# Optimization experiments

Hardware: AMD Instinct MI355X
Metric: run time of the kernel (lower is better)

The kernel has to match this reference:

```python
import jax, jax.numpy as jnp
import numpy as np

EPS = 1e-5      # batch-norm epsilon
ALPHA = 0.2     # leaky_relu negative slope


def bn_lrelu(h, gamma, beta):
    # training-mode batch norm over the batch axis, then leaky relu
    mean = jnp.mean(h, axis=0)
    var = jnp.var(h, axis=0)
    h = (h - mean) * jax.lax.rsqrt(var + EPS) * gamma + beta
    return jnp.where(h >= 0, h, ALPHA * h)


def setup_inputs() -> dict:
    key = jax.random.key(0)
    ks = jax.random.split(key, 16)
    O, T, Din, H, Dout = 50000, 200000, 128, 512, 128
    s = 0.02
    inp = {
        "obj_vecs": jax.random.normal(ks[0], (O, Din), jnp.float32),
        "pred_vecs": jax.random.normal(ks[1], (T, Din), jnp.float32),
        "edges": jax.random.randint(ks[2], (T, 2), 0, O, jnp.int64),
        # net1: [3*Din -> H -> 2H+Dout], each Linear followed by BN + leaky_relu
        "W1a": jax.random.normal(ks[3], (3 * Din, H), jnp.float32) * s,
        "b1a": jnp.zeros((H,), jnp.float32),
        "g1a": jnp.ones((H,), jnp.float32),
        "be1a": jnp.zeros((H,), jnp.float32),
        "W1b": jax.random.normal(ks[4], (H, 2 * H + Dout), jnp.float32) * s,
        "b1b": jnp.zeros((2 * H + Dout,), jnp.float32),
        "g1b": jnp.ones((2 * H + Dout,), jnp.float32),
        "be1b": jnp.zeros((2 * H + Dout,), jnp.float32),
        # net2: [H -> H -> Dout]
        "W2a": jax.random.normal(ks[5], (H, H), jnp.float32) * s,
        "b2a": jnp.zeros((H,), jnp.float32),
        "g2a": jnp.ones((H,), jnp.float32),
        "be2a": jnp.zeros((H,), jnp.float32),
        "W2b": jax.random.normal(ks[6], (H, Dout), jnp.float32) * s,
        "b2b": jnp.zeros((Dout,), jnp.float32),
        "g2b": jnp.ones((Dout,), jnp.float32),
        "be2b": jnp.zeros((Dout,), jnp.float32),
    }
    return inp


def reference(obj_vecs, pred_vecs, edges,
              W1a, b1a, g1a, be1a, W1b, b1b, g1b, be1b,
              W2a, b2a, g2a, be2a, W2b, b2b, g2b, be2b):
    O = obj_vecs.shape[0]
    H = W1a.shape[1]
    Dout = W2b.shape[1]
    s_idx = edges[:, 0]
    o_idx = edges[:, 1]

    # gather subject/object vecs and concat with predicate vecs: [T, 3*Din]
    cur_t = jnp.concatenate([obj_vecs[s_idx], pred_vecs, obj_vecs[o_idx]], axis=1)

    # net1 MLP
    h = bn_lrelu(cur_t @ W1a + b1a, g1a, be1a)           # [T, H]
    new_t = bn_lrelu(h @ W1b + b1b, g1b, be1b)            # [T, 2H+Dout]

    new_s = new_t[:, :H]
    new_p = new_t[:, H:H + Dout]
    new_o = new_t[:, H + Dout:]

    # scatter-add pooling back to objects, then average
    pooled = jnp.zeros((O, H), jnp.float32).at[s_idx].add(new_s).at[o_idx].add(new_o)
    counts = jnp.zeros((O,), jnp.float32).at[s_idx].add(1.0).at[o_idx].add(1.0)
    counts = jnp.clip(counts, 1.0, float(O))
    pooled = pooled / counts[:, None]

    # net2 MLP
    h2 = bn_lrelu(pooled @ W2a + b2a, g2a, be2a)          # [O, H]
    new_obj = bn_lrelu(h2 @ W2b + b2b, g2b, be2b)         # [O, Dout]
    return new_obj, new_p
```

## Files before the change

### kernel.cpp

```cpp
#include <hip/hip_runtime.h>

typedef __bf16 bf16;
typedef __bf16 bf16x8 __attribute__((ext_vector_type(8)));
typedef float  f32x4  __attribute__((ext_vector_type(4)));

#define BM 128
#define BN 128
#define BKT 64
#define LDK (BKT + 8)
#define LDT 72

template<int AMODE, int EPI>
__global__ __launch_bounds__(256) void gemm_k(
    const bf16* __restrict__ Abf, const float* __restrict__ Af32,
    const float* __restrict__ obj, const float* __restrict__ pred,
    const int* __restrict__ edges, const float* __restrict__ invcnt,
    const float* __restrict__ scale, const float* __restrict__ shift,
    const float* __restrict__ oscale, const float* __restrict__ oshift,
    const bf16* __restrict__ WT,
    bf16* __restrict__ outB, float* __restrict__ outF,
    float* __restrict__ pooled, float* __restrict__ gsum, float* __restrict__ gsq,
    int M, int N, int K)
{
  __shared__ __align__(16) bf16 As[BM][LDK];
  __shared__ __align__(16) bf16 Bs[BN][LDK];
  __shared__ float sc_sh[(AMODE == 1) ? 512 : 1];
  __shared__ float sh_sh[(AMODE == 1) ? 512 : 1];
  __shared__ float osc[(EPI == 2) ? BN : 1];
  __shared__ float osh[(EPI == 2) ? BN : 1];
  __shared__ int eS[(AMODE == 0 || EPI == 2) ? BM : 1];
  __shared__ int eO[(AMODE == 0 || EPI == 2) ? BM : 1];

  const int tid = threadIdx.x;
  const int m0 = blockIdx.y * BM;
  const int n0 = blockIdx.x * BN;
  const int lane = tid & 63;
  const int w = tid >> 6;
  const int wm = (w >> 1) * 64;
  const int wn = (w & 1) * 64;
  const int l15 = lane & 15;
  const int quad = lane >> 4;

  if (AMODE == 1) {
    for (int c = tid; c < K; c += 256) { sc_sh[c] = scale[c]; sh_sh[c] = shift[c]; }
  }
  if (EPI == 2) {
    if (tid < BN) { osc[tid] = oscale[n0 + tid]; osh[tid] = oshift[n0 + tid]; }
  }
  if (AMODE == 0 || EPI == 2) {
    if (tid < BM) {
      int r = m0 + tid; if (r >= M) r = M - 1;
      eS[tid] = edges[2 * r];
      eO[tid] = edges[2 * r + 1];
    }
  }
  __syncthreads();

  f32x4 acc[4][4];
  #pragma unroll
  for (int i = 0; i < 4; ++i)
    #pragma unroll
    for (int j = 0; j < 4; ++j)
      acc[i][j] = (f32x4){0.f, 0.f, 0.f, 0.f};

  for (int k0 = 0; k0 < K; k0 += BKT) {
    {
      int idx = tid;
      #pragma unroll
      for (int it = 0; it < 4; ++it, idx += 256) {
        int r = idx >> 3, c8 = (idx & 7) << 3;
        bf16x8 v = *reinterpret_cast<const bf16x8*>(WT + (size_t)(n0 + r) * K + k0 + c8);
        *reinterpret_cast<bf16x8*>(&Bs[r][c8]) = v;
      }
    }
    if (AMODE == 1 || AMODE == 3) {
      int idx = tid;
      #pragma unroll
      for (int it = 0; it < 4; ++it, idx += 256) {
        int r = idx >> 3, c8 = (idx & 7) << 3;
        int row = m0 + r; if (row >= M) row = M - 1;
        bf16x8 v = *reinterpret_cast<const bf16x8*>(Abf + (size_t)row * K + k0 + c8);
        if (AMODE == 1) {
          bf16x8 o;
          #pragma unroll
          for (int e = 0; e < 8; ++e) {
            int c = k0 + c8 + e;
            float f = sc_sh[c] * (float)v[e] + sh_sh[c];
            f = f >= 0.f ? f : 0.2f * f;
            o[e] = (bf16)f;
          }
          *reinterpret_cast<bf16x8*>(&As[r][c8]) = o;
        } else {
          *reinterpret_cast<bf16x8*>(&As[r][c8]) = v;
        }
      }
    } else {
      int idx = tid;
      #pragma unroll
      for (int it = 0; it < 8; ++it, idx += 256) {
        int r = idx >> 4, c4 = (idx & 15) << 2;
        int row = m0 + r; if (row >= M) row = M - 1;
        const float* src;
        float mul = 1.f;
        if (AMODE == 0) {
          int k = k0 + c4;
          if (k < 128)      src = obj  + (size_t)eS[r] * 128 + k;
          else if (k < 256) src = pred + (size_t)row * 128 + (k - 128);
          else              src = obj  + (size_t)eO[r] * 128 + (k - 256);
        } else {
          src = Af32 + (size_t)row * K + k0 + c4;
          mul = invcnt[row];
        }
        float4 v = *reinterpret_cast<const float4*>(src);
        As[r][c4 + 0] = (bf16)(v.x * mul);
// ... 11 lines not shown
        af[i] = *reinterpret_cast<const bf16x8*>(&As[wm + i * 16 + l15][kk + quad * 8]);
      #pragma unroll
      for (int j = 0; j < 4; ++j)
        bfv[j] = *reinterpret_cast<const bf16x8*>(&Bs[wn + j * 16 + l15][kk + quad * 8]);
      #pragma unroll
      for (int i = 0; i < 4; ++i)
        #pragma unroll
        for (int j = 0; j < 4; ++j)
          acc[i][j] = __builtin_amdgcn_mfma_f32_16x16x32_bf16(af[i], bfv[j], acc[i][j], 0, 0, 0);
    }
    __syncthreads();
  }

  if (EPI == 2) {
    #pragma unroll
    for (int i = 0; i < 4; ++i) {
      #pragma unroll
      for (int r = 0; r < 4; ++r) {
        int lrow = wm + i * 16 + quad * 4 + r;
        int row = m0 + lrow;
        if (row >= M) continue;
        #pragma unroll
        for (int j = 0; j < 4; ++j) {
          int cl = wn + j * 16 + l15;
          int n1 = n0 + cl;
          float v = osc[cl] * acc[i][j][r] + osh[cl];
          v = v >= 0.f ? v : 0.2f * v;
          if (n1 < 512)      atomicAdd(&pooled[(size_t)eS[lrow] * 512 + n1], v);
          else if (n1 < 640) outF[(size_t)row * 128 + (n1 - 512)] = v;
          else               atomicAdd(&pooled[(size_t)eO[lrow] * 512 + (n1 - 640)], v);
        }
      }
    }
  } else {
    #pragma unroll
    for (int j = 0; j < 4; ++j) {
      float s = 0.f, q = 0.f;
      #pragma unroll
      for (int i = 0; i < 4; ++i) {
        #pragma unroll
        for (int r = 0; r < 4; ++r) {
          int row = m0 + wm + i * 16 + quad * 4 + r;
          if (row >= M) continue;
          float v = acc[i][j][r];
          s += v; q += v * v;
          int col = n0 + wn + j * 16 + l15;
          if (EPI == 0) outB[(size_t)row * N + col] = (bf16)v;
          if (EPI == 3) outF[(size_t)row * N + col] = v;
        }
      }
      s += __shfl_xor(s, 16); q += __shfl_xor(q, 16);
      s += __shfl_xor(s, 32); q += __shfl_xor(q, 32);
      if (quad == 0) {
        int col = n0 + wn + j * 16 + l15;
        atomicAdd(&gsum[col], s);
        atomicAdd(&gsq[col], q);
      }
    }
  }
}

__global__ __launch_bounds__(256) void gram_k(const bf16* __restrict__ A2,
                                              float* __restrict__ G, int T) {
  __shared__ __align__(16) bf16 Ks[2][128][LDT];
  const int tid = threadIdx.x;
  const int tile = blockIdx.x & 15;
  const int s    = blockIdx.x >> 4;
  const int NS   = gridDim.x >> 4;
  const int k1b = tile >> 2, k2b = tile & 3;
  const int lane = tid & 63;
  const int w = tid >> 6;
  const int wm = (w >> 1) * 64;
  const int wn = (w & 1) * 64;
  const int l15 = lane & 15;
  const int quad = lane >> 4;

  const int NG = (T + 63) >> 6;
  const int GPB = (NG + NS - 1) / NS;
  const int g0 = s * GPB;
  const int gend = min(NG, g0 + GPB);

  f32x4 acc[4][4];
  #pragma unroll
  for (int i = 0; i < 4; ++i)
    #pragma unroll
    for (int j = 0; j < 4; ++j)
      acc[i][j] = (f32x4){0.f, 0.f, 0.f, 0.f};

  const int bsel = (k1b == k2b) ? 0 : 1;

  for (int g = g0; g < gend; ++g) {
    const int t0 = g << 6;
    #pragma unroll
    for (int it = 0; it < 4; ++it) {
      int lin = it * 256 + tid;
      int t = lin >> 4, c8 = lin & 15;
      int row = t0 + t;
      bf16x8 v;
      #pragma unroll
      for (int e = 0; e < 8; ++e) v[e] = (bf16)0.f;
      if (row < T)
        v = *reinterpret_cast<const bf16x8*>(A2 + (size_t)row * 512 + k1b * 128 + c8 * 8);
// ... 20 lines not shown
    __syncthreads();
    #pragma unroll
    for (int kk = 0; kk < 64; kk += 32) {
      bf16x8 af[4], bfv[4];
      #pragma unroll
      for (int i = 0; i < 4; ++i) {
        int r = wm + i * 16 + l15;
        int toff = (kk + quad * 8) ^ (((r >> 3) & 7) << 3);
        af[i] = *reinterpret_cast<const bf16x8*>(&Ks[0][r][toff]);
      }
      #pragma unroll
      for (int j = 0; j < 4; ++j) {
        int r = wn + j * 16 + l15;
        int toff = (kk + quad * 8) ^ (((r >> 3) & 7) << 3);
        bfv[j] = *reinterpret_cast<const bf16x8*>(&Ks[bsel][r][toff]);
      }
      #pragma unroll
      for (int i = 0; i < 4; ++i)
        #pragma unroll
        for (int j = 0; j < 4; ++j)
          acc[i][j] = __builtin_amdgcn_mfma_f32_16x16x32_bf16(af[i], bfv[j], acc[i][j], 0, 0, 0);
    }
    __syncthreads();
  }

  #pragma unroll
  for (int i = 0; i < 4; ++i) {
    #pragma unroll
    for (int r = 0; r < 4; ++r) {
      int grow = k1b * 128 + wm + i * 16 + quad * 4 + r;
      #pragma unroll
      for (int j = 0; j < 4; ++j) {
        int gcol = k2b * 128 + wn + j * 16 + l15;
        atomicAdd(&G[(size_t)grow * 512 + gcol], acc[i][j][r]);
      }
    }
  }
}

__global__ __launch_bounds__(256) void act_colsum_k(bf16* __restrict__ hA,
    const float* __restrict__ scale, const float* __restrict__ shift,
    float* __restrict__ csum, int T) {
  __shared__ float sh[4 * 512];
  const int tid = threadIdx.x;
  const int c0 = (tid & 63) * 8;
  const int rofs = tid >> 6;
  float sc[8], sf[8];
  #pragma unroll
  for (int j = 0; j < 8; ++j) { sc[j] = scale[c0 + j]; sf[j] = shift[c0 + j]; }
  float acc[8];
  #pragma unroll
  for (int j = 0; j < 8; ++j) acc[j] = 0.f;
  for (int r = blockIdx.x * 4 + rofs; r < T; r += gridDim.x * 4) {
    bf16x8 v = *reinterpret_cast<const bf16x8*>(hA + (size_t)r * 512 + c0);
    bf16x8 o;
    #pragma unroll
    for (int j = 0; j < 8; ++j) {
      float f = sc[j] * (float)v[j] + sf[j];
      f = f >= 0.f ? f : 0.2f * f;
      o[j] = (bf16)f;
      acc[j] += (float)o[j];
    }
    *reinterpret_cast<bf16x8*>(hA + (size_t)r * 512 + c0) = o;
  }
  #pragma unroll
  for (int j = 0; j < 8; ++j) sh[rofs * 512 + c0 + j] = acc[j];
  __syncthreads();
// ... 41 lines not shown
    #pragma unroll
    for (int c = 0; c < 4; ++c) { rq[w][c] = pq[c]; rs[w][c] = ps[c]; }
  }
  __syncthreads();
  if (tid < 4) {
    sqB[c0 + tid]  = rq[0][tid] + rq[1][tid] + rq[2][tid] + rq[3][tid];
    sumB[c0 + tid] = rs[0][tid] + rs[1][tid] + rs[2][tid] + rs[3][tid];
  }
}

__global__ __launch_bounds__(256) void tconv_k(const float* __restrict__ W,
                                               bf16* __restrict__ WT, int K, int N) {
  int idx = blockIdx.x * 256 + threadIdx.x;
  if (idx < K * N) {
    int n = idx / K, k = idx - n * K;
    WT[(size_t)n * K + k] = (bf16)W[(size_t)k * N + n];
  }
}

__global__ __launch_bounds__(256) void bnfin_k(const float* __restrict__ sum,
    const float* __restrict__ sq, const float* __restrict__ g,
    const float* __restrict__ be, float* __restrict__ scale,
    float* __restrict__ shift, int C, float invR) {
  int c = blockIdx.x * 256 + threadIdx.x;
  if (c < C) {
    float m = sum[c] * invR;
    float v = sq[c] * invR - m * m;
    float a = g[c] * rsqrtf(v + 1e-5f);
    scale[c] = a;
    shift[c] = be[c] - m * a;
  }
}

__global__ __launch_bounds__(256) void cntint_k(const int* __restrict__ edges,
                                                int* __restrict__ cnt, int T) {
  int t = blockIdx.x * 256 + threadIdx.x;
  if (t < T) {
    atomicAdd(&cnt[edges[2 * t]], 1);
    atomicAdd(&cnt[edges[2 * t + 1]], 1);
  }
}

__global__ __launch_bounds__(256) void invcnt_k(const int* __restrict__ cnt,
                                                float* __restrict__ invc, int O) {
  int i = blockIdx.x * 256 + threadIdx.x;
  if (i < O) {
    float c = fminf(fmaxf((float)cnt[i], 1.f), (float)O);
    invc[i] = 1.f / c;
  }
}

__global__ __launch_bounds__(1024) void scan_k(const int* __restrict__ cnt,
    int* __restrict__ rowptr, int* __restrict__ head, int O, int total) {
  __shared__ int sh[1024];
  const int t = threadIdx.x;
  const int C = (O + 1023) / 1024;
  const int i0 = t * C;
  int s = 0;
  for (int i = 0; i < C; ++i) { int idx = i0 + i; if (idx < O) s += cnt[idx]; }
  sh[t] = s;
  __syncthreads();
  for (int d = 1; d < 1024; d <<= 1) {
    int v = (t >= d) ? sh[t - d] : 0;
    __syncthreads();
    sh[t] += v;
    __syncthreads();
  }
  int run = (t == 0) ? 0 : sh[t - 1];
  for (int i = 0; i < C; ++i) {
    int idx = i0 + i;
    if (idx < O) { rowptr[idx] = run; head[idx] = run; run += cnt[idx]; }
  }
  if (t == 0) rowptr[O] = total;
}

__global__ __launch_bounds__(256) void fill_k(const int* __restrict__ edges,
    int* __restrict__ head, int* __restrict__ list, int T) {
  int t = blockIdx.x * 256 + threadIdx.x;
  if (t < T) {
    int s = edges[2 * t];
    int p = atomicAdd(&head[s], 1);
    list[p] = t << 1;
    int o = edges[2 * t + 1];
    p = atomicAdd(&head[o], 1);
    list[p] = (t << 1) | 1;
  }
}

__global__ __launch_bounds__(256) void act_k(bf16* __restrict__ hA,
    const float* __restrict__ scale, const float* __restrict__ shift, size_t n8) {
  size_t i = (size_t)blockIdx.x * 256 + threadIdx.x;
  if (i < n8) {
    size_t idx8 = i * 8;
    int c = (int)(idx8 & 511);
    bf16x8 v = *reinterpret_cast<const bf16x8*>(hA + idx8);
    bf16x8 o;
    #pragma unroll
    for (int j = 0; j < 8; ++j) {
      float f = scale[c + j] * (float)v[j] + shift[c + j];
      f = f >= 0.f ? f : 0.2f * f;
      o[j] = (bf16)f;
    }
    *reinterpret_cast<bf16x8*>(hA + idx8) = o;
  }
}

__global__ __launch_bounds__(256) void newp_k(const bf16* __restrict__ tB,
    const float* __restrict__ scale, const float* __restrict__ shift,
    float* __restrict__ outP, int T) {
  int i = blockIdx.x * 256 + threadIdx.x;
  if (i < T * 128) {
    int t = i >> 7, c = i & 127;
    float v = scale[512 + c] * (float)tB[(size_t)t * 1152 + 512 + c] + shift[512 + c];
    outP[i] = v >= 0.f ? v : 0.2f * v;
  }
}

__global__ __launch_bounds__(256) void gather_k(const bf16* __restrict__ tB,
    const int* __restrict__ rowptr, const int* __restrict__ list,
    const float* __restrict__ scale, const float* __restrict__ shift,
    const float* __restrict__ invc, bf16* __restrict__ pooled, int O) {
  int o = blockIdx.x * 4 + (threadIdx.x >> 6);
  if (o >= O) return;
  int lane = threadIdx.x & 63;
  int c0 = lane * 8;
  float scS[8], shS[8], scO[8], shO[8];
  #pragma unroll
  for (int j = 0; j < 8; ++j) {
    scS[j] = scale[c0 + j];       shS[j] = shift[c0 + j];
    scO[j] = scale[640 + c0 + j]; shO[j] = shift[640 + c0 + j];
  }
  float acc[8];
  #pragma unroll
  for (int j = 0; j < 8; ++j) acc[j] = 0.f;
  int e0 = rowptr[o], e1 = rowptr[o + 1];
  for (int e = e0; e < e1; ++e) {
    int id = list[e];
    int t = id >> 1;
    int role = id & 1;
    const bf16* row = tB + (size_t)t * 1152 + (role ? 640 : 0) + c0;
    bf16x8 v = *reinterpret_cast<const bf16x8*>(row);
    if (role) {
      #pragma unroll
      for (int j = 0; j < 8; ++j) {
        float f = scO[j] * (float)v[j] + shO[j];
        acc[j] += (f >= 0.f ? f : 0.2f * f);
      }
    } else {
      #pragma unroll
      for (int j = 0; j < 8; ++j) {
        float f = scS[j] * (float)v[j] + shS[j];
        acc[j] += (f >= 0.f ? f : 0.2f * f);
      }
    }
  }
  float ic = invc[o];
  bf16x8 out;
  #pragma unroll
  for (int j = 0; j < 8; ++j) out[j] = (bf16)(acc[j] * ic);
  *reinterpret_cast<bf16x8*>(pooled + (size_t)o * 512 + c0) = out;
}

__global__ __launch_bounds__(256) void final_k(float* __restrict__ buf,
    const float* __restrict__ scale, const float* __restrict__ shift, int n) {
  int i = blockIdx.x * 256 + threadIdx.x;
  if (i < n) {
    int c = i & 127;
    float v = scale[c] * buf[i] + shift[c];
    buf[i] = v >= 0.f ? v : 0.2f * v;
  }
}

extern "C" void kernel_launch(void* const* d_in, const int* in_sizes, int n_in,
                              void* d_out, int out_size, void* d_ws, size_t ws_size,
                              hipStream_t stream) {
  const float* obj   = (const float*)d_in[0];
  const float* pred  = (const float*)d_in[1];
  const int*   edges = (const int*)d_in[2];
  const float* W1a = (const float*)d_in[3];
  const float* g1a = (const float*)d_in[5];
  const float* be1a= (const float*)d_in[6];
  const float* W1b = (const float*)d_in[7];
  const float* g1b = (const float*)d_in[9];
  const float* be1b= (const float*)d_in[10];
  const float* W2a = (const float*)d_in[11];
  const float* g2a = (const float*)d_in[13];
  const float* be2a= (const float*)d_in[14];
  const float* W2b = (const float*)d_in[15];
  const float* g2b = (const float*)d_in[17];
  const float* be2b= (const float*)d_in[18];

  const int O = in_sizes[0] / 128;
  const int T = in_sizes[1] / 128;
  float* out_obj = (float*)d_out;
  float* out_p   = (float*)d_out + (size_t)O * 128;

  char* base = (char*)d_ws;
  size_t off = 0;
  auto alloc = [&](size_t bytes) { size_t p = off; off += (bytes + 255) & ~(size_t)255; return p; };
  size_t oWT1a = alloc((size_t)384 * 512 * 2);
  size_t oWT1b = alloc((size_t)512 * 1152 * 2);
  size_t oWT2a = alloc((size_t)512 * 512 * 2);
  size_t oWT2b = alloc((size_t)512 * 128 * 2);
  size_t oSums = alloc(4608 * 4);
  size_t oScl  = alloc(4608 * 4);
  size_t oG    = alloc((size_t)512 * 512 * 4);
  size_t oCsum = alloc(512 * 4);
  size_t oCntI = alloc((size_t)O * 4);
  size_t oInvc = alloc((size_t)O * 4);
  size_t oRp   = alloc((size_t)(O + 1) * 4);
  size_t oHead = alloc((size_t)O * 4);
  size_t oList = alloc((size_t)2 * T * 4);
  size_t oHA   = alloc((size_t)T * 512 * 2);
  size_t oBig  = off;
  size_t need_staged = oBig + (((size_t)T * 1152 * 2 + 255) & ~(size_t)255)
                            + (size_t)O * 512 * 2;
  const bool staged = (ws_size >= need_staged);

  bf16* WT1a = (bf16*)(base + oWT1a);
  bf16* WT1b = (bf16*)(base + oWT1b);
  bf16* WT2a = (bf16*)(base + oWT2a);
  bf16* WT2b = (bf16*)(base + oWT2b);
  float* sums = (float*)(base + oSums);
  float* sumA = sums,        * sqA = sums + 512;
  float* sumB = sums + 1024, * sqB = sums + 2176;
  float* sumC = sums + 3328, * sqC = sums + 3840;
  float* sumD = sums + 4352, * sqD = sums + 4480;
  float* scl = (float*)(base + oScl);
  float* scaleA = scl,        * shiftA = scl + 512;
  float* scaleB = scl + 1024, * shiftB = scl + 2176;
  float* scaleC = scl + 3328, * shiftC = scl + 3840;
  float* scaleD = scl + 4352, * shiftD = scl + 4480;
  float* Gm   = (float*)(base + oG);
  float* csum = (float*)(base + oCsum);
  int*   cntI = (int*)(base + oCntI);
  float* invc = (float*)(base + oInvc);
  int*   rowptr = (int*)(base + oRp);
  int*   head = (int*)(base + oHead);
  int*   list = (int*)(base + oList);
  bf16*  hA = (bf16*)(base + oHA);
  bf16*  h2 = (bf16*)(base + oHA);
  bf16*  tB = (bf16*)(base + oBig);
  bf16*  pooledB = (bf16*)(base + oBig + (((size_t)T * 1152 * 2 + 255) & ~(size_t)255));
  float* pooledF = (float*)(base + oBig);
  float* objpre = out_obj;

  hipMemsetAsync(sums, 0, 4608 * 4, stream);
  hipMemsetAsync(cntI, 0, (size_t)O * 4, stream);
  if (!staged) {
    hipMemsetAsync(Gm, 0, (size_t)512 * 512 * 4, stream);
    hipMemsetAsync(csum, 0, 512 * 4, stream);
  }

  tconv_k<<<(384 * 512 + 255) / 256, 256, 0, stream>>>(W1a, WT1a, 384, 512);
  tconv_k<<<(512 * 1152 + 255) / 256, 256, 0, stream>>>(W1b, WT1b, 512, 1152);
  tconv_k<<<(512 * 512 + 255) / 256, 256, 0, stream>>>(W2a, WT2a, 512, 512);
  tconv_k<<<(512 * 128 + 255) / 256, 256, 0, stream>>>(W2b, WT2b, 512, 128);
  cntint_k<<<(T + 255) / 256, 256, 0, stream>>>(edges, cntI, T);
  invcnt_k<<<(O + 255) / 256, 256, 0, stream>>>(cntI, invc, O);
  if (staged) {
    scan_k<<<1, 1024, 0, stream>>>(cntI, rowptr, head, O, 2 * T);
    fill_k<<<(T + 255) / 256, 256, 0, stream>>>(edges, head, list, T);
  }

  const int Tb = (T + BM - 1) / BM;
  const int Ob = (O + BM - 1) / BM;

  {
    dim3 g(512 / BN, Tb);
    gemm_k<0, 0><<<g, 256, 0, stream>>>(nullptr, nullptr, obj, pred, edges, nullptr,
        nullptr, nullptr, nullptr, nullptr, WT1a, hA, nullptr, nullptr, sumA, sqA,
        T, 512, 384);
  }
  bnfin_k<<<2, 256, 0, stream>>>(sumA, sqA, g1a, be1a, scaleA, shiftA, 512, 1.f / T);

  if (staged) {
    act_k<<<(int)(((size_t)T * 512 / 8 + 255) / 256), 256, 0, stream>>>(hA, scaleA,
        shiftA, (size_t)T * 512 / 8);
    {
      dim3 g(1152 / BN, Tb);
      gemm_k<3, 0><<<g, 256, 0, stream>>>(hA, nullptr, nullptr, nullptr, nullptr, nullptr,
          nullptr, nullptr, nullptr, nullptr, WT1b, tB, nullptr, nullptr, sumB, sqB,
          T, 1152, 512);
    }
    bnfin_k<<<5, 256, 0, stream>>>(sumB, sqB, g1b, be1b, scaleB, shiftB, 1152, 1.f / T);

    newp_k<<<(T * 128 + 255) / 256, 256, 0, stream>>>(tB, scaleB, shiftB, out_p, T);
    gather_k<<<(O + 3) / 4, 256, 0, stream>>>(tB, rowptr, list, scaleB, shiftB, invc,
        pooledB, O);

    {
      dim3 g(512 / BN, Ob);
      gemm_k<3, 0><<<g, 256, 0, stream>>>(pooledB, nullptr, nullptr, nullptr, nullptr,
          nullptr, nullptr, nullptr, nullptr, nullptr, WT2a, h2, nullptr, nullptr,
          sumC, sqC, O, 512, 512);
    }
  } else {
    hipMemsetAsync(pooledF, 0, (size_t)O * 512 * 4, stream);
    act_colsum_k<<<1024, 256, 0, stream>>>(hA, scaleA, shiftA, csum, T);
    gram_k<<<512, 256, 0, stream>>>(hA, Gm, T);
    colstat_k<<<288, 256, 0, stream>>>(Gm, csum, W1b, sumB, sqB);
    bnfin_k<<<5, 256, 0, stream>>>(sumB, sqB, g1b, be1b, scaleB, shiftB, 1152, 1.f / T);
    {
      dim3 g(1152 / BN, Tb);
      gemm_k<3, 2><<<g, 256, 0, stream>>>(hA, nullptr, nullptr, nullptr, edges, nullptr,
          nullptr, nullptr, scaleB, shiftB, WT1b, nullptr, out_p, pooledF, nullptr,
          nullptr, T, 1152, 512);
    }
    {
      dim3 g(512 / BN, Ob);
      gemm_k<2, 0><<<g, 256, 0, stream>>>(nullptr, pooledF, nullptr, nullptr, nullptr,
          invc, nullptr, nullptr, nullptr, nullptr, WT2a, h2, nullptr, nullptr,
          sumC, sqC, O, 512, 512);
    }
  }
  bnfin_k<<<2, 256, 0, stream>>>(sumC, sqC, g2a, be2a, scaleC, shiftC, 512, 1.f / O);

  {
    dim3 g(128 / BN, Ob);
    gemm_k<1, 3><<<g, 256, 0, stream>>>(h2, nullptr, nullptr, nullptr, nullptr, nullptr,
        scaleC, shiftC, nullptr, nullptr, WT2b, nullptr, objpre, nullptr, sumD, sqD,
        O, 128, 512);
  }
  bnfin_k<<<1, 256, 0, stream>>>(sumD, sqD, g2b, be2b, scaleD, shiftD, 128, 1.f / O);

  final_k<<<((size_t)O * 128 + 255) / 256, 256, 0, stream>>>(objpre, scaleD, shiftD,
      (int)((size_t)O * 128));
}
```

Before: 2.189 ms.

## Replace atomic scatter pooling with sorted-permutation GEMM and segmented reduction; symmetric Gram

In the non-staged path, edges are sorted by subject and by object via counting sort. The second net1 GEMM then reads hA rows in permuted order, writes bf16 activated rows to a chunk buffer, and a segment kernel sums contiguous rows per object into pooled without atomics. This aims to remove the heavy float atomicAdd scatter to pooled, at the cost of extra passes, a chunked buffer and splitting the GEMM into two launches. The Gram kernel also computes only the upper-triangular tiles and mirrors them, dropping redundant MFMA work but adding extra atomics.

Measured after the change: 2.265 ms. +3.5%, slower.

```diff
diff --git a/kernel.cpp b/kernel.cpp
--- a/kernel.cpp
+++ b/kernel.cpp
@@ -20,19 +20,20 @@
     const bf16* __restrict__ WT,
     bf16* __restrict__ outB, float* __restrict__ outF,
     float* __restrict__ pooled, float* __restrict__ gsum, float* __restrict__ gsq,
-    int M, int N, int K)
+    int M, int N, int K,
+    const int* __restrict__ perm, int rbase)
 {
   __shared__ __align__(16) bf16 As[BM][LDK];
   __shared__ __align__(16) bf16 Bs[BN][LDK];
   __shared__ float sc_sh[(AMODE == 1) ? 512 : 1];
   __shared__ float sh_sh[(AMODE == 1) ? 512 : 1];
-  __shared__ float osc[(EPI == 2) ? BN : 1];
-  __shared__ float osh[(EPI == 2) ? BN : 1];
-  __shared__ int eS[(AMODE == 0 || EPI == 2) ? BM : 1];
+  __shared__ float osc[(EPI == 2 || EPI == 4) ? BN : 1];
+  __shared__ float osh[(EPI == 2 || EPI == 4) ? BN : 1];
+  __shared__ int eS[(AMODE == 0 || EPI == 2 || EPI == 4) ? BM : 1];
   __shared__ int eO[(AMODE == 0 || EPI == 2) ? BM : 1];
 
   const int tid = threadIdx.x;
-  const int m0 = blockIdx.y * BM;
+  const int m0 = rbase + blockIdx.y * BM;
   const int n0 = blockIdx.x * BN;
   const int lane = tid & 63;
   const int w = tid >> 6;
@@ -44,7 +45,7 @@
   if (AMODE == 1) {
     for (int c = tid; c < K; c += 256) { sc_sh[c] = scale[c]; sh_sh[c] = shift[c]; }
   }
-  if (EPI == 2) {
+  if (EPI == 2 || EPI == 4) {
     if (tid < BN) { osc[tid] = oscale[n0 + tid]; osh[tid] = oshift[n0 + tid]; }
   }
   if (AMODE == 0 || EPI == 2) {
@@ -54,6 +55,12 @@
       eO[tid] = edges[2 * r + 1];
     }
   }
+  if (EPI == 4) {
+    if (tid < BM) {
+      int r = m0 + tid; if (r >= M) r = M - 1;
+      eS[tid] = perm[r];
+    }
+  }
   __syncthreads();
 
   f32x4 acc[4][4];
@@ -73,13 +80,14 @@
         *reinterpret_cast<bf16x8*>(&Bs[r][c8]) = v;
       }
     }
-    if (AMODE == 1 || AMODE == 3) {
+    if (AMODE == 1 || AMODE == 3 || AMODE == 4) {
       int idx = tid;
       #pragma unroll
       for (int it = 0; it < 4; ++it, idx += 256) {
         int r = idx >> 3, c8 = (idx & 7) << 3;
         int row = m0 + r; if (row >= M) row = M - 1;
-        bf16x8 v = *reinterpret_cast<const bf16x8*>(Abf + (size_t)row * K + k0 + c8);
+        size_t srow = (AMODE == 4) ? (size_t)eS[r] : (size_t)row;
+        bf16x8 v = *reinterpret_cast<const bf16x8*>(Abf + srow * K + k0 + c8);
         if (AMODE == 1) {
           bf16x8 o;
           #pragma unroll
@@ -157,6 +165,25 @@
         }
       }
     }
+  } else if (EPI == 4) {
+    #pragma unroll
+    for (int i = 0; i < 4; ++i) {
+      #pragma unroll
+      for (int r = 0; r < 4; ++r) {
+        int lrow = wm + i * 16 + quad * 4 + r;
+        int row = m0 + lrow;
+        if (row >= M) continue;
+        #pragma unroll
+        for (int j = 0; j < 4; ++j) {
+          int cl = wn + j * 16 + l15;
+          int n1 = n0 + cl;
+          float v = osc[cl] * acc[i][j][r] + osh[cl];
+          v = v >= 0.f ? v : 0.2f * v;
+          if (n1 < 512) outB[(size_t)(row - rbase) * 512 + n1] = (bf16)v;
+          else          outF[(size_t)eS[lrow] * 128 + (n1 - 512)] = v;
+        }
+      }
+    }
   } else {
     #pragma unroll
     for (int j = 0; j < 4; ++j) {
@@ -185,14 +212,44 @@
   }
 }
 
+__global__ __launch_bounds__(256) void gseg_k(const bf16* __restrict__ buf,
+    const int* __restrict__ rowptr, float* __restrict__ pooled,
+    int rbase, int rend, int O) {
+  int o = blockIdx.x * 4 + (threadIdx.x >> 6);
+  if (o >= O) return;
+  int e0 = rowptr[o], e1 = rowptr[o + 1];
+  int s = e0 > rbase ? e0 : rbase;
+  int e = e1 < rend ? e1 : rend;
+  if (s >= e) return;
+  int lane = threadIdx.x & 63;
+  int c0 = lane * 8;
+  float acc[8];
+  #pragma unroll
+  for (int j = 0; j < 8; ++j) acc[j] = 0.f;
+  for (int r = s; r < e; ++r) {
+    bf16x8 v = *reinterpret_cast<const bf16x8*>(buf + (size_t)(r - rbase) * 512 + c0);
+    #pragma unroll
+    for (int j = 0; j < 8; ++j) acc[j] += (float)v[j];
+  }
+  float* dst = pooled + (size_t)o * 512 + c0;
+  float4 a = *reinterpret_cast<float4*>(dst);
+  float4 b = *reinterpret_cast<float4*>(dst + 4);
+  a.x += acc[0]; a.y += acc[1]; a.z += acc[2]; a.w += acc[3];
+  b.x += acc[4]; b.y += acc[5]; b.z += acc[6]; b.w += acc[7];
+  *reinterpret_cast<float4*>(dst) = a;
+  *reinterpret_cast<float4*>(dst + 4) = b;
+}
+
 __global__ __launch_bounds__(256) void gram_k(const bf16* __restrict__ A2,
                                               float* __restrict__ G, int T) {
   __shared__ __align__(16) bf16 Ks[2][128][LDT];
   const int tid = threadIdx.x;
-  const int tile = blockIdx.x & 15;
-  const int s    = blockIdx.x >> 4;
-  const int NS   = gridDim.x >> 4;
-  const int k1b = tile >> 2, k2b = tile & 3;
+  const int tile = blockIdx.x % 10;
+  const int s    = blockIdx.x / 10;
+  const int NS   = gridDim.x / 10;
+  const int K1T[10] = {0, 0, 0, 0, 1, 1, 1, 2, 2, 3};
+  const int K2T[10] = {0, 1, 2, 3, 1, 2, 3, 2, 3, 3};
+  const int k1b = K1T[tile], k2b = K2T[tile];
   const int lane = tid & 63;
   const int w = tid >> 6;
   const int wm = (w >> 1) * 64;
@@ -279,7 +336,10 @@
       #pragma unroll
       for (int j = 0; j < 4; ++j) {
         int gcol = k2b * 128 + wn + j * 16 + l15;
-        atomicAdd(&G[(size_t)grow * 512 + gcol], acc[i][j][r]);
+        float v = acc[i][j][r];
+        atomicAdd(&G[(size_t)grow * 512 + gcol], v);
+        if (k1b != k2b)
+          atomicAdd(&G[(size_t)gcol * 512 + grow], v);
       }
     }
   }
@@ -387,32 +447,36 @@
   }
 }
 
-__global__ __launch_bounds__(256) void cntint_k(const int* __restrict__ edges,
-                                                int* __restrict__ cnt, int T) {
+__global__ __launch_bounds__(256) void cnt2_k(const int* __restrict__ edges,
+    int* __restrict__ cntS, int* __restrict__ cntO, int T) {
   int t = blockIdx.x * 256 + threadIdx.x;
   if (t < T) {
-    atomicAdd(&cnt[edges[2 * t]], 1);
-    atomicAdd(&cnt[edges[2 * t + 1]], 1);
-  }
-}
-
-__global__ __launch_bounds__(256) void invcnt_k(const int* __restrict__ cnt,
-                                                float* __restrict__ invc, int O) {
+    atomicAdd(&cntS[edges[2 * t]], 1);
+    atomicAdd(&cntO[edges[2 * t + 1]], 1);
+  }
+}
+
+__global__ __launch_bounds__(256) void invcnt2_k(const int* __restrict__ cntS,
+    const int* __restrict__ cntO, float* __restrict__ invc, int O) {
   int i = blockIdx.x * 256 + threadIdx.x;
   if (i < O) {
-    float c = fminf(fmaxf((float)cnt[i], 1.f), (float)O);
+    float c = fminf(fmaxf((float)(cntS[i] + cntO[i]), 1.f), (float)O);
     invc[i] = 1.f / c;
   }
 }
 
-__global__ __launch_bounds__(1024) void scan_k(const int* __restrict__ cnt,
+__global__ __launch_bounds__(1024) void scan_k(const int* __restrict__ cntA,
+    const int* __restrict__ cntB,
     int* __restrict__ rowptr, int* __restrict__ head, int O, int total) {
   __shared__ int sh[1024];
   const int t = threadIdx.x;
   const int C = (O + 1023) / 1024;
   const int i0 = t * C;
   int s = 0;
-  for (int i = 0; i < C; ++i) { int idx = i0 + i; if (idx < O) s += cnt[idx]; }
+  for (int i = 0; i < C; ++i) {
+    int idx = i0 + i;
+    if (idx < O) s += cntA[idx] + (cntB ? cntB[idx] : 0);
+  }
   sh[t] = s;
   __syncthreads();
   for (int d = 1; d < 1024; d <<= 1) {
@@ -424,7 +488,11 @@
   int run = (t == 0) ? 0 : sh[t - 1];
   for (int i = 0; i < C; ++i) {
     int idx = i0 + i;
-    if (idx < O) { rowptr[idx] = run; head[idx] = run; run += cnt[idx]; }
+    if (idx < O) {
+      rowptr[idx] = run;
+      head[idx] = run;
+      run += cntA[idx] + (cntB ? cntB[idx] : 0);
+    }
   }
   if (t == 0) rowptr[O] = total;
 }
@@ -439,6 +507,20 @@
     int o = edges[2 * t + 1];
     p = atomicAdd(&head[o], 1);
     list[p] = (t << 1) | 1;
+  }
+}
+
+__global__ __launch_bounds__(256) void fill2_k(const int* __restrict__ edges,
+    int* __restrict__ headS, int* __restrict__ headO,
+    int* __restrict__ permS, int* __restrict__ permO, int T) {
+  int t = blockIdx.x * 256 + threadIdx.x;
+  if (t < T) {
+    int s = edges[2 * t];
+    int p = atomicAdd(&headS[s], 1);
+    permS[p] = t;
+    int o = edges[2 * t + 1];
+    int q = atomicAdd(&headO[o], 1);
+    permO[q] = t;
   }
 }
 
@@ -561,16 +643,33 @@
   size_t oScl  = alloc(4608 * 4);
   size_t oG    = alloc((size_t)512 * 512 * 4);
   size_t oCsum = alloc(512 * 4);
-  size_t oCntI = alloc((size_t)O * 4);
+  size_t oCntS = alloc((size_t)O * 4);
+  size_t oCntO = alloc((size_t)O * 4);
   size_t oInvc = alloc((size_t)O * 4);
-  size_t oRp   = alloc((size_t)(O + 1) * 4);
-  size_t oHead = alloc((size_t)O * 4);
+  size_t oRpS  = alloc((size_t)(O + 1) * 4);
+  size_t oRpO  = alloc((size_t)(O + 1) * 4);
+  size_t oHdS  = alloc((size_t)O * 4);
+  size_t oHdO  = alloc((size_t)O * 4);
+  size_t oPmS  = alloc((size_t)T * 4);
+  size_t oPmO  = alloc((size_t)T * 4);
   size_t oList = alloc((size_t)2 * T * 4);
   size_t oHA   = alloc((size_t)T * 512 * 2);
   size_t oBig  = off;
+
   size_t need_staged = oBig + (((size_t)T * 1152 * 2 + 255) & ~(size_t)255)
                             + (size_t)O * 512 * 2;
   const bool staged = (ws_size >= need_staged);
+
+  size_t oPool = oBig;
+  size_t oBuf  = oPool + (((size_t)O * 512 * 4 + 255) & ~(size_t)255);
+  int chunkT = 0;
+  if (!staged && ws_size > oBuf) {
+    size_t avail = ws_size - oBuf;
+    size_t ct = avail / ((size_t)512 * 2);
+    if (ct > (size_t)T) ct = T;
+    chunkT = (int)(ct & ~(size_t)127);
+  }
+  const bool sorted = (!staged && chunkT >= 4096);
 
   bf16* WT1a = (bf16*)(base + oWT1a);
   bf16* WT1b = (bf16*)(base + oWT1b);
@@ -588,34 +687,46 @@
   float* scaleD = scl + 4352, * shiftD = scl + 4480;
   float* Gm   = (float*)(base + oG);
   float* csum = (float*)(base + oCsum);
-  int*   cntI = (int*)(base + oCntI);
+  int*   cntS = (int*)(base + oCntS);
+  int*   cntO = (int*)(base + oCntO);
   float* invc = (float*)(base + oInvc);
-  int*   rowptr = (int*)(base + oRp);
-  int*   head = (int*)(base + oHead);
+  int*   rpS  = (int*)(base + oRpS);
+  int*   rpO  = (int*)(base + oRpO);
+  int*   hdS  = (int*)(base + oHdS);
+  int*   hdO  = (int*)(base + oHdO);
+  int*   permS= (int*)(base + oPmS);
+  int*   permO= (int*)(base + oPmO);
   int*   list = (int*)(base + oList);
   bf16*  hA = (bf16*)(base + oHA);
   bf16*  h2 = (bf16*)(base + oHA);
   bf16*  tB = (bf16*)(base + oBig);
   bf16*  pooledB = (bf16*)(base + oBig + (((size_t)T * 1152 * 2 + 255) & ~(size_t)255));
-  float* pooledF = (float*)(base + oBig);
+  float* pooledF = (float*)(base + oPool);
+  bf16*  bufS = (bf16*)(base + oBuf);
   float* objpre = out_obj;
 
   hipMemsetAsync(sums, 0, 4608 * 4, stream);
-  hipMemsetAsync(cntI, 0, (size_t)O * 4, stream);
+  hipMemsetAsync(cntS, 0, (size_t)O * 4, stream);
+  hipMemsetAsync(cntO, 0, (size_t)O * 4, stream);
   if (!staged) {
     hipMemsetAsync(Gm, 0, (size_t)512 * 512 * 4, stream);
     hipMemsetAsync(csum, 0, 512 * 4, stream);
+    hipMemsetAsync(pooledF, 0, (size_t)O * 512 * 4, stream);
   }
 
   tconv_k<<<(384 * 512 + 255) / 256, 256, 0, stream>>>(W1a, WT1a, 384, 512);
   tconv_k<<<(512 * 1152 + 255) / 256, 256, 0, stream>>>(W1b, WT1b, 512, 1152);
   tconv_k<<<(512 * 512 + 255) / 256, 256, 0, stream>>>(W2a, WT2a, 512, 512);
   tconv_k<<<(512 * 128 + 255) / 256, 256, 0, stream>>>(W2b, WT2b, 512, 128);
-  cntint_k<<<(T + 255) / 256, 256, 0, stream>>>(edges, cntI, T);
-  invcnt_k<<<(O + 255) / 256, 256, 0, stream>>>(cntI, invc, O);
+  cnt2_k<<<(T + 255) / 256, 256, 0, stream>>>(edges, cntS, cntO, T);
+  invcnt2_k<<<(O + 255) / 256, 256, 0, stream>>>(cntS, cntO, invc, O);
   if (staged) {
-    scan_k<<<1, 1024, 0, stream>>>(cntI, rowptr, head, O, 2 * T);
-    fill_k<<<(T + 255) / 256, 256, 0, stream>>>(edges, head, list, T);
+    scan_k<<<1, 1024, 0, stream>>>(cntS, cntO, rpS, hdS, O, 2 * T);
+    fill_k<<<(T + 255) / 256, 256, 0, stream>>>(edges, hdS, list, T);
+  } else if (sorted) {
+    scan_k<<<1, 1024, 0, stream>>>(cntS, nullptr, rpS, hdS, O, T);
+    scan_k<<<1, 1024, 0, stream>>>(cntO, nullptr, rpO, hdO, O, T);
+    fill2_k<<<(T + 255) / 256, 256, 0, stream>>>(edges, hdS, hdO, permS, permO, T);
   }
 
   const int Tb = (T + BM - 1) / BM;
@@ -625,7 +736,7 @@
     dim3 g(512 / BN, Tb);
     gemm_k<0, 0><<<g, 256, 0, stream>>>(nullptr, nullptr, obj, pred, edges, nullptr,
         nullptr, nullptr, nullptr, nullptr, WT1a, hA, nullptr, nullptr, sumA, sqA,
-        T, 512, 384);
+        T, 512, 384, nullptr, 0);
   }
   bnfin_k<<<2, 256, 0, stream>>>(sumA, sqA, g1a, be1a, scaleA, shiftA, 512, 1.f / T);
 
@@ -636,37 +747,53 @@
       dim3 g(1152 / BN, Tb);
       gemm_k<3, 0><<<g, 256, 0, stream>>>(hA, nullptr, nullptr, nullptr, nullptr, nullptr,
           nullptr, nullptr, nullptr, nullptr, WT1b, tB, nullptr, nullptr, sumB, sqB,
-          T, 1152, 512);
+          T, 1152, 512, nullptr, 0);
     }
     bnfin_k<<<5, 256, 0, stream>>>(sumB, sqB, g1b, be1b, scaleB, shiftB, 1152, 1.f / T);
-
     newp_k<<<(T * 128 + 255) / 256, 256, 0, stream>>>(tB, scaleB, shiftB, out_p, T);
-    gather_k<<<(O + 3) / 4, 256, 0, stream>>>(tB, rowptr, list, scaleB, shiftB, invc,
+    gather_k<<<(O + 3) / 4, 256, 0, stream>>>(tB, rpS, list, scaleB, shiftB, invc,
         pooledB, O);
-
     {
       dim3 g(512 / BN, Ob);
       gemm_k<3, 0><<<g, 256, 0, stream>>>(pooledB, nullptr, nullptr, nullptr, nullptr,
           nullptr, nullptr, nullptr, nullptr, nullptr, WT2a, h2, nullptr, nullptr,
-          sumC, sqC, O, 512, 512);
+          sumC, sqC, O, 512, 512, nullptr, 0);
     }
   } else {
-    hipMemsetAsync(pooledF, 0, (size_t)O * 512 * 4, stream);
     act_colsum_k<<<1024, 256, 0, stream>>>(hA, scaleA, shiftA, csum, T);
-    gram_k<<<512, 256, 0, stream>>>(hA, Gm, T);
+    gram_k<<<10 * 48, 256, 0, stream>>>(hA, Gm, T);
     colstat_k<<<288, 256, 0, stream>>>(Gm, csum, W1b, sumB, sqB);
     bnfin_k<<<5, 256, 0, stream>>>(sumB, sqB, g1b, be1b, scaleB, shiftB, 1152, 1.f / T);
-    {
+
+    if (sorted) {
+      for (int c0 = 0; c0 < T; c0 += chunkT) {
+        int c1 = min(T, c0 + chunkT);
+        dim3 g(5, (c1 - c0 + BM - 1) / BM);
+        gemm_k<4, 4><<<g, 256, 0, stream>>>(hA, nullptr, nullptr, nullptr, nullptr,
+            nullptr, nullptr, nullptr, scaleB, shiftB, WT1b, bufS, out_p, nullptr,
+            nullptr, nullptr, c1, 640, 512, permS, c0);
+        gseg_k<<<(O + 3) / 4, 256, 0, stream>>>(bufS, rpS, pooledF, c0, c1, O);
+      }
+      for (int c0 = 0; c0 < T; c0 += chunkT) {
+        int c1 = min(T, c0 + chunkT);
+        dim3 g(4, (c1 - c0 + BM - 1) / BM);
+        gemm_k<4, 4><<<g, 256, 0, stream>>>(hA, nullptr, nullptr, nullptr, nullptr,
+            nullptr, nullptr, nullptr, scaleB + 640, shiftB + 640,
+            WT1b + (size_t)640 * 512, bufS, out_p, nullptr,
+            nullptr, nullptr, c1, 512, 512, permO, c0);
+        gseg_k<<<(O + 3) / 4, 256, 0, stream>>>(bufS, rpO, pooledF, c0, c1, O);
+      }
+    } else {
       dim3 g(1152 / BN, Tb);
       gemm_k<3, 2><<<g, 256, 0, stream>>>(hA, nullptr, nullptr, nullptr, edges, nullptr,
           nullptr, nullptr, scaleB, shiftB, WT1b, nullptr, out_p, pooledF, nullptr,
-          nullptr, T, 1152, 512);
+          nullptr, T, 1152, 512, nullptr, 0);
     }
     {
       dim3 g(512 / BN, Ob);
       gemm_k<2, 0><<<g, 256, 0, stream>>>(nullptr, pooledF, nullptr, nullptr, nullptr,
           invc, nullptr, nullptr, nullptr, nullptr, WT2a, h2, nullptr, nullptr,
-          sumC, sqC, O, 512, 512);
+          sumC, sqC, O, 512, 512, nullptr, 0);
     }
   }
   bnfin_k<<<2, 256, 0, stream>>>(sumC, sqC, g2a, be2a, scaleC, shiftC, 512, 1.f / O);
@@ -675,7 +802,7 @@
     dim3 g(128 / BN, Ob);
     gemm_k<1, 3><<<g, 256, 0, stream>>>(h2, nullptr, nullptr, nullptr, nullptr, nullptr,
         scaleC, shiftC, nullptr, nullptr, WT2b, nullptr, objpre, nullptr, sumD, sqD,
-        O, 128, 512);
+        O, 128, 512, nullptr, 0);
   }
   bnfin_k<<<1, 256, 0, stream>>>(sumD, sqD, g2b, be2b, scaleD, shiftD, 128, 1.f / O);
 
```

## Chunk net1 second GEMM with fused BN epilogue and deterministic gather pooling

Applied to the files above, without the earlier changes.

The staged path used to run act_k and a full bf16 GEMM writing the pre-activation tB, then newp_k and gather_k. It now always derives layer-B BN statistics from the Gram matrix, and computes only the upper-triangle tiles of the Gram matrix, mirroring off-diagonal results. The second GEMM then runs in workspace-sized row chunks with a fused BN+lrelu epilogue writing bf16 s/o slices. A CSR gather adds each chunk into fp32 pooled sums, replacing the atomics and extra passes over a large intermediate. It also adds a grouped block-index swizzle for L2 reuse in every GEMM, at the cost of more kernel launches and repeated CSR scans per chunk.

New measurement: 2.226 ms. No clear change (+1.7%).

```diff
diff --git a/kernel.cpp b/kernel.cpp
--- a/kernel.cpp
+++ b/kernel.cpp
@@ -20,20 +20,40 @@
     const bf16* __restrict__ WT,
     bf16* __restrict__ outB, float* __restrict__ outF,
     float* __restrict__ pooled, float* __restrict__ gsum, float* __restrict__ gsq,
-    int M, int N, int K)
+    int M, int N, int K, int rbase)
 {
   __shared__ __align__(16) bf16 As[BM][LDK];
   __shared__ __align__(16) bf16 Bs[BN][LDK];
   __shared__ float sc_sh[(AMODE == 1) ? 512 : 1];
   __shared__ float sh_sh[(AMODE == 1) ? 512 : 1];
-  __shared__ float osc[(EPI == 2) ? BN : 1];
-  __shared__ float osh[(EPI == 2) ? BN : 1];
+  __shared__ float osc[(EPI == 2 || EPI == 5) ? BN : 1];
+  __shared__ float osh[(EPI == 2 || EPI == 5) ? BN : 1];
   __shared__ int eS[(AMODE == 0 || EPI == 2) ? BM : 1];
   __shared__ int eO[(AMODE == 0 || EPI == 2) ? BM : 1];
 
   const int tid = threadIdx.x;
-  const int m0 = blockIdx.y * BM;
-  const int n0 = blockIdx.x * BN;
+
+  int bx = blockIdx.x, by = blockIdx.y;
+  {
+    const int NX = gridDim.x, NY = gridDim.y;
+    int L = by * NX + bx;
+    int bpg = NX * 8;
+    int nFull = NY >> 3;
+    int Lfull = nFull * bpg;
+    if (L < Lfull) {
+      int g = L / bpg, w2 = L - g * bpg;
+      by = (g << 3) + (w2 & 7);
+      bx = w2 >> 3;
+    } else {
+      int r2 = L - Lfull;
+      int q = r2 / NX;
+      by = (nFull << 3) + q;
+      bx = r2 - q * NX;
+    }
+  }
+  const int m0 = rbase + by * BM;
+  const int n0 = bx * BN;
+
   const int lane = tid & 63;
   const int w = tid >> 6;
   const int wm = (w >> 1) * 64;
@@ -44,7 +64,7 @@
   if (AMODE == 1) {
     for (int c = tid; c < K; c += 256) { sc_sh[c] = scale[c]; sh_sh[c] = shift[c]; }
   }
-  if (EPI == 2) {
+  if (EPI == 2 || EPI == 5) {
     if (tid < BN) { osc[tid] = oscale[n0 + tid]; osh[tid] = oshift[n0 + tid]; }
   }
   if (AMODE == 0 || EPI == 2) {
@@ -157,6 +177,26 @@
         }
       }
     }
+  } else if (EPI == 5) {
+    #pragma unroll
+    for (int i = 0; i < 4; ++i) {
+      #pragma unroll
+      for (int r = 0; r < 4; ++r) {
+        int lrow = wm + i * 16 + quad * 4 + r;
+        int row = m0 + lrow;
+        if (row >= M) continue;
+        #pragma unroll
+        for (int j = 0; j < 4; ++j) {
+          int cl = wn + j * 16 + l15;
+          int n1 = n0 + cl;
+          float v = osc[cl] * acc[i][j][r] + osh[cl];
+          v = v >= 0.f ? v : 0.2f * v;
+          if (n1 < 512)      outB[(size_t)(row - rbase) * 1024 + n1] = (bf16)v;
+          else if (n1 < 640) outF[(size_t)row * 128 + (n1 - 512)] = v;
+          else               outB[(size_t)(row - rbase) * 1024 + (n1 - 128)] = (bf16)v;
+        }
+      }
+    }
   } else {
     #pragma unroll
     for (int j = 0; j < 4; ++j) {
@@ -185,14 +225,48 @@
   }
 }
 
+__global__ __launch_bounds__(256) void gatherc_k(const bf16* __restrict__ buf,
+    const int* __restrict__ rowptr, const int* __restrict__ list,
+    float* __restrict__ pooled, int c0, int c1, int O) {
+  int o = blockIdx.x * 4 + (threadIdx.x >> 6);
+  if (o >= O) return;
+  int lane = threadIdx.x & 63;
+  int cc = lane * 8;
+  int e0 = rowptr[o], e1 = rowptr[o + 1];
+  float acc[8];
+  #pragma unroll
+  for (int j = 0; j < 8; ++j) acc[j] = 0.f;
+  bool any = false;
+  for (int e = e0; e < e1; ++e) {
+    int id = list[e];
+    int t = id >> 1;
+    if (t < c0 || t >= c1) continue;
+    const bf16* row = buf + (size_t)(t - c0) * 1024 + (id & 1) * 512 + cc;
+    bf16x8 v = *reinterpret_cast<const bf16x8*>(row);
+    #pragma unroll
+    for (int j = 0; j < 8; ++j) acc[j] += (float)v[j];
+    any = true;
+  }
+  if (!any) return;
+  float* dst = pooled + (size_t)o * 512 + cc;
+  float4 a = *reinterpret_cast<float4*>(dst);
+  float4 b = *reinterpret_cast<float4*>(dst + 4);
+  a.x += acc[0]; a.y += acc[1]; a.z += acc[2]; a.w += acc[3];
+  b.x += acc[4]; b.y += acc[5]; b.z += acc[6]; b.w += acc[7];
+  *reinterpret_cast<float4*>(dst) = a;
+  *reinterpret_cast<float4*>(dst + 4) = b;
+}
+
 __global__ __launch_bounds__(256) void gram_k(const bf16* __restrict__ A2,
                                               float* __restrict__ G, int T) {
   __shared__ __align__(16) bf16 Ks[2][128][LDT];
   const int tid = threadIdx.x;
-  const int tile = blockIdx.x & 15;
-  const int s    = blockIdx.x >> 4;
-  const int NS   = gridDim.x >> 4;
-  const int k1b = tile >> 2, k2b = tile & 3;
+  const int tile = blockIdx.x % 10;
+  const int s    = blockIdx.x / 10;
+  const int NS   = gridDim.x / 10;
+  const int K1T[10] = {0, 0, 0, 0, 1, 1, 1, 2, 2, 3};
+  const int K2T[10] = {0, 1, 2, 3, 1, 2, 3, 2, 3, 3};
+  const int k1b = K1T[tile], k2b = K2T[tile];
   const int lane = tid & 63;
   const int w = tid >> 6;
   const int wm = (w >> 1) * 64;
@@ -279,7 +353,10 @@
       #pragma unroll
       for (int j = 0; j < 4; ++j) {
         int gcol = k2b * 128 + wn + j * 16 + l15;
-        atomicAdd(&G[(size_t)grow * 512 + gcol], acc[i][j][r]);
+        float v = acc[i][j][r];
+        atomicAdd(&G[(size_t)grow * 512 + gcol], v);
+        if (k1b != k2b)
+          atomicAdd(&G[(size_t)gcol * 512 + grow], v);
       }
     }
   }
@@ -440,80 +517,6 @@
     p = atomicAdd(&head[o], 1);
     list[p] = (t << 1) | 1;
   }
-}
-
-__global__ __launch_bounds__(256) void act_k(bf16* __restrict__ hA,
-    const float* __restrict__ scale, const float* __restrict__ shift, size_t n8) {
-  size_t i = (size_t)blockIdx.x * 256 + threadIdx.x;
-  if (i < n8) {
-    size_t idx8 = i * 8;
-    int c = (int)(idx8 & 511);
-    bf16x8 v = *reinterpret_cast<const bf16x8*>(hA + idx8);
-    bf16x8 o;
-    #pragma unroll
-    for (int j = 0; j < 8; ++j) {
-      float f = scale[c + j] * (float)v[j] + shift[c + j];
-      f = f >= 0.f ? f : 0.2f * f;
-      o[j] = (bf16)f;
-    }
-    *reinterpret_cast<bf16x8*>(hA + idx8) = o;
-  }
-}
-
-__global__ __launch_bounds__(256) void newp_k(const bf16* __restrict__ tB,
-    const float* __restrict__ scale, const float* __restrict__ shift,
-    float* __restrict__ outP, int T) {
-  int i = blockIdx.x * 256 + threadIdx.x;
-  if (i < T * 128) {
-    int t = i >> 7, c = i & 127;
-    float v = scale[512 + c] * (float)tB[(size_t)t * 1152 + 512 + c] + shift[512 + c];
-    outP[i] = v >= 0.f ? v : 0.2f * v;
-  }
-}
-
-__global__ __launch_bounds__(256) void gather_k(const bf16* __restrict__ tB,
-    const int* __restrict__ rowptr, const int* __restrict__ list,
-    const float* __restrict__ scale, const float* __restrict__ shift,
-    const float* __restrict__ invc, bf16* __restrict__ pooled, int O) {
-  int o = blockIdx.x * 4 + (threadIdx.x >> 6);
-  if (o >= O) return;
-  int lane = threadIdx.x & 63;
-  int c0 = lane * 8;
-  float scS[8], shS[8], scO[8], shO[8];
-  #pragma unroll
-  for (int j = 0; j < 8; ++j) {
-    scS[j] = scale[c0 + j];       shS[j] = shift[c0 + j];
-    scO[j] = scale[640 + c0 + j]; shO[j] = shift[640 + c0 + j];
-  }
-  float acc[8];
-  #pragma unroll
-  for (int j = 0; j < 8; ++j) acc[j] = 0.f;
-  int e0 = rowptr[o], e1 = rowptr[o + 1];
-  for (int e = e0; e < e1; ++e) {
-    int id = list[e];
-    int t = id >> 1;
-    int role = id & 1;
-    const bf16* row = tB + (size_t)t * 1152 + (role ? 640 : 0) + c0;
-    bf16x8 v = *reinterpret_cast<const bf16x8*>(row);
-    if (role) {
-      #pragma unroll
-      for (int j = 0; j < 8; ++j) {
-        float f = scO[j] * (float)v[j] + shO[j];
-        acc[j] += (f >= 0.f ? f : 0.2f * f);
-      }
-    } else {
-      #pragma unroll
-      for (int j = 0; j < 8; ++j) {
-        float f = scS[j] * (float)v[j] + shS[j];
-        acc[j] += (f >= 0.f ? f : 0.2f * f);
-      }
-    }
-  }
-  float ic = invc[o];
-  bf16x8 out;
-  #pragma unroll
-  for (int j = 0; j < 8; ++j) out[j] = (bf16)(acc[j] * ic);
-  *reinterpret_cast<bf16x8*>(pooled + (size_t)o * 512 + c0) = out;
 }
 
 __global__ __launch_bounds__(256) void final_k(float* __restrict__ buf,
@@ -561,16 +564,22 @@
   size_t oScl  = alloc(4608 * 4);
   size_t oG    = alloc((size_t)512 * 512 * 4);
   size_t oCsum = alloc(512 * 4);
-  size_t oCntI = alloc((size_t)O * 4);
+  size_t oCnt  = alloc((size_t)O * 4);
   size_t oInvc = alloc((size_t)O * 4);
   size_t oRp   = alloc((size_t)(O + 1) * 4);
   size_t oHead = alloc((size_t)O * 4);
   size_t oList = alloc((size_t)2 * T * 4);
   size_t oHA   = alloc((size_t)T * 512 * 2);
-  size_t oBig  = off;
-  size_t need_staged = oBig + (((size_t)T * 1152 * 2 + 255) & ~(size_t)255)
-                            + (size_t)O * 512 * 2;
-  const bool staged = (ws_size >= need_staged);
+  size_t oPool = off;
+  size_t oBuf  = oPool + (((size_t)O * 512 * 4 + 255) & ~(size_t)255);
+
+  int chunkT = 0;
+  if (ws_size > oBuf) {
+    size_t ct = (ws_size - oBuf) / 2048;
+    if (ct > (size_t)T) ct = T;
+    chunkT = (int)(ct & ~(size_t)127);
+  }
+  const bool chunked = (chunkT >= 8192);
 
   bf16* WT1a = (bf16*)(base + oWT1a);
   bf16* WT1b = (bf16*)(base + oWT1b);
@@ -588,24 +597,22 @@
   float* scaleD = scl + 4352, * shiftD = scl + 4480;
   float* Gm   = (float*)(base + oG);
   float* csum = (float*)(base + oCsum);
-  int*   cntI = (int*)(base + oCntI);
+  int*   cntI = (int*)(base + oCnt);
   float* invc = (float*)(base + oInvc);
   int*   rowptr = (int*)(base + oRp);
   int*   head = (int*)(base + oHead);
   int*   list = (int*)(base + oList);
   bf16*  hA = (bf16*)(base + oHA);
   bf16*  h2 = (bf16*)(base + oHA);
-  bf16*  tB = (bf16*)(base + oBig);
-  bf16*  pooledB = (bf16*)(base + oBig + (((size_t)T * 1152 * 2 + 255) & ~(size_t)255));
-  float* pooledF = (float*)(base + oBig);
+  float* pooledF = (float*)(base + oPool);
+  bf16*  buf = (bf16*)(base + oBuf);
   float* objpre = out_obj;
 
   hipMemsetAsync(sums, 0, 4608 * 4, stream);
   hipMemsetAsync(cntI, 0, (size_t)O * 4, stream);
-  if (!staged) {
-    hipMemsetAsync(Gm, 0, (size_t)512 * 512 * 4, stream);
-    hipMemsetAsync(csum, 0, 512 * 4, stream);
-  }
+  hipMemsetAsync(Gm, 0, (size_t)512 * 512 * 4, stream);
+  hipMemsetAsync(csum, 0, 512 * 4, stream);
+  hipMemsetAsync(pooledF, 0, (size_t)O * 512 * 4, stream);
 
   tconv_k<<<(384 * 512 + 255) / 256, 256, 0, stream>>>(W1a, WT1a, 384, 512);
   tconv_k<<<(512 * 1152 + 255) / 256, 256, 0, stream>>>(W1b, WT1b, 512, 1152);
@@ -613,7 +620,7 @@
   tconv_k<<<(512 * 128 + 255) / 256, 256, 0, stream>>>(W2b, WT2b, 512, 128);
   cntint_k<<<(T + 255) / 256, 256, 0, stream>>>(edges, cntI, T);
   invcnt_k<<<(O + 255) / 256, 256, 0, stream>>>(cntI, invc, O);
-  if (staged) {
+  if (chunked) {
     scan_k<<<1, 1024, 0, stream>>>(cntI, rowptr, head, O, 2 * T);
     fill_k<<<(T + 255) / 256, 256, 0, stream>>>(edges, head, list, T);
   }
@@ -625,49 +632,36 @@
     dim3 g(512 / BN, Tb);
     gemm_k<0, 0><<<g, 256, 0, stream>>>(nullptr, nullptr, obj, pred, edges, nullptr,
         nullptr, nullptr, nullptr, nullptr, WT1a, hA, nullptr, nullptr, sumA, sqA,
-        T, 512, 384);
+        T, 512, 384, 0);
   }
   bnfin_k<<<2, 256, 0, stream>>>(sumA, sqA, g1a, be1a, scaleA, shiftA, 512, 1.f / T);
 
-  if (staged) {
-    act_k<<<(int)(((size_t)T * 512 / 8 + 255) / 256), 256, 0, stream>>>(hA, scaleA,
-        shiftA, (size_t)T * 512 / 8);
-    {
-      dim3 g(1152 / BN, Tb);
-      gemm_k<3, 0><<<g, 256, 0, stream>>>(hA, nullptr, nullptr, nullptr, nullptr, nullptr,
-          nullptr, nullptr, nullptr, nullptr, WT1b, tB, nullptr, nullptr, sumB, sqB,
-          T, 1152, 512);
-    }
-    bnfin_k<<<5, 256, 0, stream>>>(sumB, sqB, g1b, be1b, scaleB, shiftB, 1152, 1.f / T);
-
-    newp_k<<<(T * 128 + 255) / 256, 256, 0, stream>>>(tB, scaleB, shiftB, out_p, T);
-    gather_k<<<(O + 3) / 4, 256, 0, stream>>>(tB, rowptr, list, scaleB, shiftB, invc,
-        pooledB, O);
-
-    {
-      dim3 g(512 / BN, Ob);
-      gemm_k<3, 0><<<g, 256, 0, stream>>>(pooledB, nullptr, nullptr, nullptr, nullptr,
-          nullptr, nullptr, nullptr, nullptr, nullptr, WT2a, h2, nullptr, nullptr,
-          sumC, sqC, O, 512, 512);
+  act_colsum_k<<<1024, 256, 0, stream>>>(hA, scaleA, shiftA, csum, T);
+  gram_k<<<10 * 48, 256, 0, stream>>>(hA, Gm, T);
+  colstat_k<<<288, 256, 0, stream>>>(Gm, csum, W1b, sumB, sqB);
+  bnfin_k<<<5, 256, 0, stream>>>(sumB, sqB, g1b, be1b, scaleB, shiftB, 1152, 1.f / T);
+
+  if (chunked) {
+    for (int c0 = 0; c0 < T; c0 += chunkT) {
+      int c1 = min(T, c0 + chunkT);
+      dim3 g(1152 / BN, (c1 - c0 + BM - 1) / BM);
+      gemm_k<3, 5><<<g, 256, 0, stream>>>(hA, nullptr, nullptr, nullptr, nullptr,
+          nullptr, nullptr, nullptr, scaleB, shiftB, WT1b, buf, out_p, nullptr,
+          nullptr, nullptr, c1, 1152, 512, c0);
+      gatherc_k<<<(O + 3) / 4, 256, 0, stream>>>(buf, rowptr, list, pooledF, c0, c1, O);
     }
   } else {
-    hipMemsetAsync(pooledF, 0, (size_t)O * 512 * 4, stream);
-    act_colsum_k<<<1024, 256, 0, stream>>>(hA, scaleA, shiftA, csum, T);
-    gram_k<<<512, 256, 0, stream>>>(hA, Gm, T);
-    colstat_k<<<288, 256, 0, stream>>>(Gm, csum, W1b, sumB, sqB);
-    bnfin_k<<<5, 256, 0, stream>>>(sumB, sqB, g1b, be1b, scaleB, shiftB, 1152, 1.f / T);
-    {
-      dim3 g(1152 / BN, Tb);
-      gemm_k<3, 2><<<g, 256, 0, stream>>>(hA, nullptr, nullptr, nullptr, edges, nullptr,
-          nullptr, nullptr, scaleB, shiftB, WT1b, nullptr, out_p, pooledF, nullptr,
-          nullptr, T, 1152, 512);
-    }
-    {
-      dim3 g(512 / BN, Ob);
-      gemm_k<2, 0><<<g, 256, 0, stream>>>(nullptr, pooledF, nullptr, nullptr, nullptr,
-          invc, nullptr, nullptr, nullptr, nullptr, WT2a, h2, nullptr, nullptr,
-          sumC, sqC, O, 512, 512);
-    }
+    dim3 g(1152 / BN, Tb);
+    gemm_k<3, 2><<<g, 256, 0, stream>>>(hA, nullptr, nullptr, nullptr, edges, nullptr,
+        nullptr, nullptr, scaleB, shiftB, WT1b, nullptr, out_p, pooledF, nullptr,
+        nullptr, T, 1152, 512, 0);
+  }
+
+  {
+    dim3 g(512 / BN, Ob);
+    gemm_k<2, 0><<<g, 256, 0, stream>>>(nullptr, pooledF, nullptr, nullptr, nullptr,
+        invc, nullptr, nullptr, nullptr, nullptr, WT2a, h2, nullptr, nullptr,
+        sumC, sqC, O, 512, 512, 0);
   }
   bnfin_k<<<2, 256, 0, stream>>>(sumC, sqC, g2a, be2a, scaleC, shiftC, 512, 1.f / O);
 
@@ -675,7 +669,7 @@
     dim3 g(128 / BN, Ob);
     gemm_k<1, 3><<<g, 256, 0, stream>>>(h2, nullptr, nullptr, nullptr, nullptr, nullptr,
         scaleC, shiftC, nullptr, nullptr, WT2b, nullptr, objpre, nullptr, sumD, sqD,
-        O, 128, 512);
+        O, 128, 512, 0);
   }
   bnfin_k<<<1, 256, 0, stream>>>(sumD, sqD, g2b, be2b, scaleD, shiftD, 128, 1.f / O);
 
```
